# Kernel tuning notes

Measured on AMD Instinct MI355X. Metric: run time of the kernel, lower is better.

Reference implementation:

```python
import jax, jax.numpy as jnp
import numpy as np

TEMPERATURE = 0.07
EPS = 1e-12  # F.normalize clamp


def _project(x, We, be, W1, b1, W2, b2):
    # encoder Linear then projection head Linear->ReLU->Linear
    h = x @ We + be                      # [B, 512]
    h = jax.nn.relu(h @ W1 + b1)         # [B, 256]
    return h @ W2 + b2                   # [B, 128]


def _ntxent(z1, z2, t):
    B = z1.shape[0]
    z1 = z1 / jnp.maximum(jnp.linalg.norm(z1, axis=1, keepdims=True), EPS)
    z2 = z2 / jnp.maximum(jnp.linalg.norm(z2, axis=1, keepdims=True), EPS)
    reps = jnp.concatenate([z1, z2], axis=0)          # [2B, 128]
    sim = reps @ reps.T                               # [2B, 2B]
    N = 2 * B
    idx = jnp.arange(N)
    # positives: eye rolled by B along columns -> column (i+B) mod N
    pos = sim[idx, (idx + B) % N][:, None]            # [N, 1]
    # negatives: all off-diagonal entries per row, in column order
    cols = jnp.arange(N - 1)[None, :]                 # [1, N-1]
    neg_idx = cols + (cols >= idx[:, None])           # skip the diagonal
    neg = jnp.take_along_axis(sim, neg_idx, axis=1)   # [N, N-1]
    logits = jnp.concatenate([pos, neg], axis=1) / t  # [N, N]
    # cross-entropy with label 0
    return jnp.mean(jax.nn.logsumexp(logits, axis=1) - logits[:, 0])


def setup_inputs() -> dict:
    key = jax.random.key(0)
    ks = jax.random.split(key, 10)
    B, Din, Denc, Dh, Dp = 4096, 1024, 512, 256, 128
    s = lambda fan_in: 1.0 / np.sqrt(fan_in)
    return {
        "x_image": jax.random.normal(ks[0], (B, Din), jnp.float32),
        "x_text": jax.random.normal(ks[1], (B, Din), jnp.float32),
        "We_img": jax.random.normal(ks[2], (Din, Denc), jnp.float32) * s(Din),
        "be_img": jnp.zeros((Denc,), jnp.float32),
        "We_txt": jax.random.normal(ks[3], (Din, Denc), jnp.float32) * s(Din),
        "be_txt": jnp.zeros((Denc,), jnp.float32),
        "Wp1_img": jax.random.normal(ks[4], (Denc, Dh), jnp.float32) * s(Denc),
        "bp1_img": jnp.zeros((Dh,), jnp.float32),
        "Wp2_img": jax.random.normal(ks[5], (Dh, Dp), jnp.float32) * s(Dh),
        "bp2_img": jnp.zeros((Dp,), jnp.float32),
        "Wp1_txt": jax.random.normal(ks[6], (Denc, Dh), jnp.float32) * s(Denc),
        "bp1_txt": jnp.zeros((Dh,), jnp.float32),
        "Wp2_txt": jax.random.normal(ks[7], (Dh, Dp), jnp.float32) * s(Dh),
        "bp2_txt": jnp.zeros((Dp,), jnp.float32),
    }


def reference(x_image, x_text, We_img, be_img, We_txt, be_txt,
              Wp1_img, bp1_img, Wp2_img, bp2_img,
              Wp1_txt, bp1_txt, Wp2_txt, bp2_txt):
    z1 = _project(x_image, We_img, be_img, Wp1_img, bp1_img, Wp2_img, bp2_img)
    z2 = _project(x_text, We_txt, be_txt, Wp1_txt, bp1_txt, Wp2_txt, bp2_txt)
    # single modality pair ('image','text') -> one NT-Xent loss
    return _ntxent(z1, z2, TEMPERATURE)
```

## Files before the change

kernel.cpp:

```cpp
#include <hip/hip_runtime.h>
#include <hip/hip_bf16.h>
#include <math.h>

typedef __bf16 bf16_t;
typedef __bf16 bf8 __attribute__((ext_vector_type(8)));
typedef __bf16 bf4 __attribute__((ext_vector_type(4)));
typedef __bf16 bf16x2 __attribute__((ext_vector_type(2)));
typedef float f32x4 __attribute__((ext_vector_type(4)));

#define AS1 __attribute__((address_space(1)))
#define AS3 __attribute__((address_space(3)))

#define B_ROWS 4096
#define NTOT   8192
#define DIN    1024
#define DENC   512
#define DH     256
#define DP     128
#define NSLICE 16
#define INV_T        14.285714285714286f
#define SCALE_LOG2   20.609929155556620f

__device__ __forceinline__ f32x4 mfma_16x16x32(bf8 a, bf8 b, f32x4 c) {
  return __builtin_amdgcn_mfma_f32_16x16x32_bf16(a, b, c, 0, 0, 0);
}

__global__ __launch_bounds__(256) void prep_kernel(
    const float* __restrict__ x_i, const float* __restrict__ x_t,
    const float* __restrict__ We_i, const float* __restrict__ We_t,
    const float* __restrict__ W1_i, const float* __restrict__ W1_t,
    const float* __restrict__ W2_i, const float* __restrict__ W2_t,
    bf16_t* __restrict__ xb_i, bf16_t* __restrict__ xb_t,
    bf16_t* __restrict__ Wet_i, bf16_t* __restrict__ Wet_t,
    bf16_t* __restrict__ W1t_i, bf16_t* __restrict__ W1t_t,
    bf16_t* __restrict__ W2t_i, bf16_t* __restrict__ W2t_t,
    int* __restrict__ Ctr) {
  const int b = blockIdx.x;
  const int tid = threadIdx.x;
  if (b >= 336) {
    int idx = (b - 336) * 256 + tid;
    const int HALF = (B_ROWS * DIN) / 4;
    const float* s; bf16_t* d; int off;
    if (idx < HALF) { s = x_i; d = xb_i; off = idx; }
    else            { s = x_t; d = xb_t; off = idx - HALF; }
    float4 v = ((const float4*)s)[off];
    bf4 w = { (bf16_t)v.x, (bf16_t)v.y, (bf16_t)v.z, (bf16_t)v.w };
    ((bf4*)d)[off] = w;
    return;
  }
  if (b == 0 && tid < 2) Ctr[tid] = 0;
  const float* src; bf16_t* dst; int K, N, tile;
  if (b < 128)      { src = We_i; dst = Wet_i; K = 1024; N = 512; tile = b; }
  else if (b < 256) { src = We_t; dst = Wet_t; K = 1024; N = 512; tile = b - 128; }
  else if (b < 288) { src = W1_i; dst = W1t_i; K = 512;  N = 256; tile = b - 256; }
  else if (b < 320) { src = W1_t; dst = W1t_t; K = 512;  N = 256; tile = b - 288; }
  else if (b < 328) { src = W2_i; dst = W2t_i; K = 256;  N = 128; tile = b - 320; }
  else              { src = W2_t; dst = W2t_t; K = 256;  N = 128; tile = b - 328; }
  const int tilesN = N >> 6;
  const int k0 = (tile / tilesN) * 64;
  const int n0 = (tile % tilesN) * 64;

  __shared__ float ld[64][65];
  #pragma unroll
  for (int i = 0; i < 4; ++i) {
    int cid = tid + i * 256;
    int r = cid >> 4;
    int c = (cid & 15) * 4;
    float4 v = *(const float4*)(src + (size_t)(k0 + r) * N + n0 + c);
    ld[r][c + 0] = v.x; ld[r][c + 1] = v.y; ld[r][c + 2] = v.z; ld[r][c + 3] = v.w;
  }
  __syncthreads();
  #pragma unroll
  for (int i = 0; i < 2; ++i) {
    int cid = tid + i * 256;
    int rn = cid >> 3;
    int c8 = (cid & 7) * 8;
    bf8 w;
    #pragma unroll
    for (int j = 0; j < 8; ++j) w[j] = (bf16_t)ld[c8 + j][rn];
    *(bf8*)(dst + (size_t)(n0 + rn) * K + k0 + c8) = w;
  }
}

template<int MT, bool RELU>
__global__ __launch_bounds__(256) void gemm_glds(
    const bf16_t* __restrict__ A0, const bf16_t* __restrict__ A1,
    const bf16_t* __restrict__ B0, const bf16_t* __restrict__ B1,
    const float* __restrict__ bias0, const float* __restrict__ bias1,
    bf16_t* __restrict__ out0, bf16_t* __restrict__ out1,
    int N, int K) {
  const bf16_t* A   = blockIdx.z ? A1 : A0;
  const bf16_t* Bt  = blockIdx.z ? B1 : B0;
  const float* bias = blockIdx.z ? bias1 : bias0;
  bf16_t* outp      = blockIdx.z ? out1 : out0;

  const int nb   = blockIdx.x * 64;
  const int mb   = blockIdx.y * MT;
  const int tid  = threadIdx.x;
  const int wave = tid >> 6;
  const int lane = tid & 63;
  const int l15  = lane & 15;
  const int quad = lane >> 4;
  constexpr int CH = MT / 64;

  __shared__ __align__(16) bf16_t As[2][MT * 32];
  __shared__ __align__(16) bf16_t Bs[2][64 * 32];

  f32x4 acc[CH][4];
  #pragma unroll
  for (int i = 0; i < CH; ++i)
    #pragma unroll
    for (int j = 0; j < 4; ++j) acc[i][j] = (f32x4){0.f, 0.f, 0.f, 0.f};

  auto stage = [&](int k0, int pb) {
    #pragma unroll
    for (int i = 0; i < CH; ++i) {
      const int s = tid + i * 256;
      const bf16_t* ga = A + (size_t)(mb + (s >> 2)) * K + k0 + (s & 3) * 8;
      __builtin_amdgcn_global_load_lds(
          (const AS1 void*)ga,
          (AS3 void*)(As[pb] + (size_t)(wave * 64 + i * 256) * 8), 16, 0, 0);
    }
    const bf16_t* gb = Bt + (size_t)(nb + (tid >> 2)) * K + k0 + (tid & 3) * 8;
    __builtin_amdgcn_global_load_lds(
        (const AS1 void*)gb,
        (AS3 void*)(Bs[pb] + (size_t)(wave * 64) * 8), 16, 0, 0);
  };

  stage(0, 0);
  const int T = K >> 5;
  for (int t = 0; t < T; ++t) {
    __syncthreads();
    if (t + 1 < T) stage((t + 1) << 5, (t + 1) & 1);
    const bf16_t* as = As[t & 1];
    const bf16_t* bs = Bs[t & 1];
    bf8 a[CH];
    #pragma unroll
    for (int i = 0; i < CH; ++i)
      a[i] = *(const bf8*)(as + (size_t)(wave * (16 * CH) + i * 16 + l15) * 32 + quad * 8);
    #pragma unroll
    for (int nt = 0; nt < 4; ++nt) {
      bf8 bb = *(const bf8*)(bs + (size_t)(nt * 16 + l15) * 32 + quad * 8);
      #pragma unroll
      for (int i = 0; i < CH; ++i)
        acc[i][nt] = mfma_16x16x32(a[i], bb, acc[i][nt]);
    }
  }

  #pragma unroll
  for (int i = 0; i < CH; ++i) {
    const int orow = mb + wave * (16 * CH) + i * 16 + quad * 4;
    #pragma unroll
    for (int nt = 0; nt < 4; ++nt) {
      const int ocol = nb + nt * 16 + l15;
      const float bval = bias[ocol];
      #pragma unroll
      for (int r = 0; r < 4; ++r) {
        float v = acc[i][nt][r] + bval;
        if (RELU) v = fmaxf(v, 0.f);
        outp[(size_t)(orow + r) * N + ocol] = (bf16_t)v;
      }
    }
  }
}

__global__ __launch_bounds__(256) void head2_norm(
    const bf16_t* __restrict__ A0, const bf16_t* __restrict__ A1,
    const bf16_t* __restrict__ B0, const bf16_t* __restrict__ B1,
    const float* __restrict__ bias0, const float* __restrict__ bias1,
    bf16_t* __restrict__ reps) {
  const bf16_t* A   = blockIdx.z ? A1 : A0;
  const bf16_t* Bt  = blockIdx.z ? B1 : B0;
  const float* bias = blockIdx.z ? bias1 : bias0;

  const int mb   = blockIdx.x * 64;
  const int tid  = threadIdx.x;
  const int wave = tid >> 6;
  const int lane = tid & 63;
  const int l15  = lane & 15;
  const int quad = lane >> 4;

  __shared__ __align__(16) bf16_t As[64][40];
  __shared__ __align__(16) bf16_t Bs[128][40];

  f32x4 acc[8];
  #pragma unroll
  for (int i = 0; i < 8; ++i) acc[i] = (f32x4){0.f, 0.f, 0.f, 0.f};

  const int arow   = tid >> 2;
  const int achunk = (tid & 3) << 3;
  const bf16_t* Ap = A + (size_t)(mb + arow) * DH + achunk;

  for (int k0 = 0; k0 < DH; k0 += 32) {
    uint4 av = *(const uint4*)(Ap + k0);
    uint4 bv[2];
    #pragma unroll
    for (int i = 0; i < 2; ++i) {
      int cid = tid + i * 256;
      int br = cid >> 2, bc = (cid & 3) << 3;
      bv[i] = *(const uint4*)(Bt + (size_t)br * DH + k0 + bc);
    }
    __syncthreads();
    *(uint4*)&As[arow][achunk] = av;
    #pragma unroll
    for (int i = 0; i < 2; ++i) {
      int cid = tid + i * 256;
      int br = cid >> 2, bc = (cid & 3) << 3;
      *(uint4*)&Bs[br][bc] = bv[i];
    }
    __syncthreads();
    bf8 af = *(const bf8*)&As[wave * 16 + l15][quad * 8];
    #pragma unroll
    for (int nt = 0; nt < 8; ++nt) {
      bf8 bfv = *(const bf8*)&Bs[nt * 16 + l15][quad * 8];
      acc[nt] = mfma_16x16x32(af, bfv, acc[nt]);
    }
  }

  #pragma unroll
  for (int nt = 0; nt < 8; ++nt) {
    const float bval = bias[nt * 16 + l15];
    #pragma unroll
    for (int r = 0; r < 4; ++r) acc[nt][r] += bval;
  }
  const size_t rowbase = (size_t)(blockIdx.z ? B_ROWS : 0) + mb + wave * 16 + quad * 4;
  #pragma unroll
  for (int r = 0; r < 4; ++r) {
    float ss = 0.f;
    #pragma unroll
    for (int nt = 0; nt < 8; ++nt) ss += acc[nt][r] * acc[nt][r];
    ss += __shfl_xor(ss, 1);
    ss += __shfl_xor(ss, 2);
    ss += __shfl_xor(ss, 4);
    ss += __shfl_xor(ss, 8);
    const float inv = 1.0f / fmaxf(sqrtf(ss), 1e-12f);
    #pragma unroll
    for (int nt = 0; nt < 8; ++nt)
      reps[(rowbase + r) * DP + nt * 16 + l15] = (bf16_t)(acc[nt][r] * inv);
  }
}

__global__ __launch_bounds__(256) void sim_rowsum_kernel(
    const bf16_t* __restrict__ reps, float* __restrict__ Spart) {
  const int rowbase = blockIdx.y * 128;
  const int slice   = blockIdx.x;
  const int col0    = slice * 512;
  const int tid  = threadIdx.x;
  const int wave = tid >> 6;
  const int lane = tid & 63;
  const int l15  = lane & 15;
  const int quad = lane >> 4;

  __shared__ __align__(16) bf16_t Bs[2][64 * DP];

  const int r0 = rowbase + wave * 32;
  bf8 af0[4], af1[4];
  #pragma unroll
  for (int kt = 0; kt < 4; ++kt) {
    af0[kt] = *(const bf8*)(reps + (size_t)(r0 + l15)      * DP + kt * 32 + quad * 8);
    af1[kt] = *(const bf8*)(reps + (size_t)(r0 + 16 + l15) * DP + kt * 32 + quad * 8);
  }

  float rs0[4] = {0.f, 0.f, 0.f, 0.f};
  float rs1[4] = {0.f, 0.f, 0.f, 0.f};

  for (int t = 0; t < 8; ++t) {
    bf16_t* buf = Bs[t & 1];
    __syncthreads();
    const int jt0 = col0 + t * 64;
    #pragma unroll
    for (int r = 0; r < 4; ++r) {
      const int s   = r * 256 + tid;
      const int col = s >> 4;
      const int cf  = (s & 15) ^ (col & 15);
      const bf16_t* g = reps + (size_t)(jt0 + col) * DP + cf * 8;
      __builtin_amdgcn_global_load_lds(
          (const AS1 void*)g,
          (AS3 void*)(buf + (size_t)(r * 256 + wave * 64) * 8), 16, 0, 0);
    }
    __syncthreads();

    #pragma unroll
    for (int st = 0; st < 4; ++st) {
      const bf16_t* base = buf + (size_t)(st * 16 + l15) * DP;
      bf8 b0 = *(const bf8*)(base + (((0 * 4 + quad) ^ l15) * 8));
      bf8 b1 = *(const bf8*)(base + (((1 * 4 + quad) ^ l15) * 8));
      bf8 b2 = *(const bf8*)(base + (((2 * 4 + quad) ^ l15) * 8));
      bf8 b3 = *(const bf8*)(base + (((3 * 4 + quad) ^ l15) * 8));
      f32x4 acc0 = (f32x4){0.f, 0.f, 0.f, 0.f};
      f32x4 acc1 = (f32x4){0.f, 0.f, 0.f, 0.f};
      acc0 = mfma_16x16x32(af0[0], b0, acc0); acc1 = mfma_16x16x32(af1[0], b0, acc1);
      acc0 = mfma_16x16x32(af0[1], b1, acc0); acc1 = mfma_16x16x32(af1[1], b1, acc1);
      acc0 = mfma_16x16x32(af0[2], b2, acc0); acc1 = mfma_16x16x32(af1[2], b2, acc1);
      acc0 = mfma_16x16x32(af0[3], b3, acc0); acc1 = mfma_16x16x32(af1[3], b3, acc1);
      #pragma unroll
      for (int r = 0; r < 4; ++r) {
        rs0[r] += __builtin_amdgcn_exp2f(acc0[r] * SCALE_LOG2);
        rs1[r] += __builtin_amdgcn_exp2f(acc1[r] * SCALE_LOG2);
      }
    }
  }

  const int i0 = r0 + quad * 4;
  #pragma unroll
  for (int r = 0; r < 4; ++r) {
    float v = rs0[r];
    v += __shfl_xor(v, 1); v += __shfl_xor(v, 2);
    v += __shfl_xor(v, 4); v += __shfl_xor(v, 8);
    if (l15 == 0) Spart[(size_t)slice * NTOT + i0 + r] = v;
  }
  #pragma unroll
  for (int r = 0; r < 4; ++r) {
    float v = rs1[r];
    v += __shfl_xor(v, 1); v += __shfl_xor(v, 2);
    v += __shfl_xor(v, 4); v += __shfl_xor(v, 8);
    if (l15 == 0) Spart[(size_t)slice * NTOT + i0 + 16 + r] = v;
  }
}

__global__ __launch_bounds__(256) void rowfinal_kernel(
    const bf16_t* __restrict__ reps, const float* __restrict__ Spart,
    int* __restrict__ cnt, float* __restrict__ Lsum,
    float* __restrict__ out) {
  const int tid  = threadIdx.x;
  const int wave = tid >> 6;
  const int lane = tid & 63;
  float part = 0.f;
  #pragma unroll 1
  for (int i = 0; i < 16; ++i) {
    const int row = blockIdx.x * 64 + wave * 16 + i;
    bf16x2 a = *(const bf16x2*)(reps + (size_t)row * DP + lane * 2);
    bf16x2 b = *(const bf16x2*)(reps + (size_t)(row ^ B_ROWS) * DP + lane * 2);
    float a0 = (float)a.x, a1 = (float)a.y;
    float b0 = (float)b.x, b1 = (float)b.y;
    float dii = a0 * a0 + a1 * a1;
    float pos = a0 * b0 + a1 * b1;
    float ps  = (lane < NSLICE) ? Spart[(size_t)lane * NTOT + row] : 0.f;
    #pragma unroll
    for (int m = 1; m < 64; m <<= 1) {
      dii += __shfl_xor(dii, m);
      pos += __shfl_xor(pos, m);
      ps  += __shfl_xor(ps, m);
    }
    if (lane == 0) {
      float Si = ps - __builtin_amdgcn_exp2f(dii * SCALE_LOG2)
                    + __builtin_amdgcn_exp2f(pos * SCALE_LOG2);
      part += logf(Si) - pos * INV_T;
    }
  }
  __shared__ float wpart[4];
  if (lane == 0) wpart[wave] = part;
  __syncthreads();
  if (tid == 0) {
    float bsum = wpart[0] + wpart[1] + wpart[2] + wpart[3];
    atomicAdd(Lsum, bsum);
    __threadfence();
    int old = __hip_atomic_fetch_add(cnt, 1, __ATOMIC_ACQ_REL,
                                     __HIP_MEMORY_SCOPE_AGENT);
    if (old == (int)gridDim.x - 1) {
      float tot = __hip_atomic_load(Lsum, __ATOMIC_RELAXED,
                                    __HIP_MEMORY_SCOPE_AGENT);
      out[0] = tot * (1.0f / NTOT);
    }
  }
}

extern "C" void kernel_launch(void* const* d_in, const int* in_sizes, int n_in,
                              void* d_out, int out_size, void* d_ws, size_t ws_size,
                              hipStream_t stream) {
  const float* x_img  = (const float*)d_in[0];
  const float* x_txt  = (const float*)d_in[1];
  const float* We_img = (const float*)d_in[2];
  const float* be_img = (const float*)d_in[3];
  const float* We_txt = (const float*)d_in[4];
  const float* be_txt = (const float*)d_in[5];
  const float* W1_img = (const float*)d_in[6];
  const float* b1_img = (const float*)d_in[7];
  const float* W2_img = (const float*)d_in[8];
  const float* b2_img = (const float*)d_in[9];
  const float* W1_txt = (const float*)d_in[10];
  const float* b1_txt = (const float*)d_in[11];
  const float* W2_txt = (const float*)d_in[12];
  const float* b2_txt = (const float*)d_in[13];

  char* p = (char*)d_ws;
  bf16_t* xbf_img = (bf16_t*)p; p += (size_t)B_ROWS * DIN * 2;
  bf16_t* xbf_txt = (bf16_t*)p; p += (size_t)B_ROWS * DIN * 2;
  bf16_t* Wet_img = (bf16_t*)p; p += (size_t)DENC * DIN * 2;
  bf16_t* Wet_txt = (bf16_t*)p; p += (size_t)DENC * DIN * 2;
  bf16_t* W1t_img = (bf16_t*)p; p += (size_t)DH * DENC * 2;
  bf16_t* W1t_txt = (bf16_t*)p; p += (size_t)DH * DENC * 2;
  bf16_t* W2t_img = (bf16_t*)p; p += (size_t)DP * DH * 2;
  bf16_t* W2t_txt = (bf16_t*)p; p += (size_t)DP * DH * 2;
  bf16_t* h_img   = (bf16_t*)p; p += (size_t)B_ROWS * DENC * 2;
  bf16_t* h_txt   = (bf16_t*)p; p += (size_t)B_ROWS * DENC * 2;
  bf16_t* g_img   = (bf16_t*)p; p += (size_t)B_ROWS * DH * 2;
  bf16_t* g_txt   = (bf16_t*)p; p += (size_t)B_ROWS * DH * 2;
  bf16_t* reps    = (bf16_t*)p; p += (size_t)NTOT * DP * 2;
  float*  Spart   = (float*) p; p += (size_t)NSLICE * NTOT * 4;
  int*    Ctr     = (int*)   p; p += 2 * 4;

  prep_kernel<<<336 + 8192, 256, 0, stream>>>(
      x_img, x_txt, We_img, We_txt, W1_img, W1_txt, W2_img, W2_txt,
      xbf_img, xbf_txt, Wet_img, Wet_txt, W1t_img, W1t_txt, W2t_img, W2t_txt,
      Ctr);

  gemm_glds<128, false><<<dim3(DENC / 64, B_ROWS / 128, 2), 256, 0, stream>>>(
      xbf_img, xbf_txt, Wet_img, Wet_txt, be_img, be_txt, h_img, h_txt,
      DENC, DIN);
  gemm_glds<64, true><<<dim3(DH / 64, B_ROWS / 64, 2), 256, 0, stream>>>(
      h_img, h_txt, W1t_img, W1t_txt, b1_img, b1_txt, g_img, g_txt,
      DH, DENC);
  head2_norm<<<dim3(B_ROWS / 64, 1, 2), 256, 0, stream>>>(
      g_img, g_txt, W2t_img, W2t_txt, b2_img, b2_txt, reps);

  sim_rowsum_kernel<<<dim3(NSLICE, NTOT / 128), 256, 0, stream>>>(reps, Spart);
  rowfinal_kernel<<<NTOT / 64, 256, 0, stream>>>(
      reps, Spart, &Ctr[0], (float*)&Ctr[1], (float*)d_out);
}
```

Baseline: 187.7 us.

## Pipeline head2 and sim loads via global_load_lds, move diag/pos corrections into sim

head2_norm now uses 16-row blocks with four times as many blocks, splits columns across waves, and stages tiles with double-buffered direct global-to-LDS loads. The row norm is reduced across waves through shared memory. sim_rowsum_kernel prefetches the next column tile while computing the current one. The diagonal and positive-pair corrections move into the sim blocks that own those columns, which writes a Pos array, so rowfinal becomes a simple per-thread sum over slices. The aim is to raise head2 parallelism, hide load latency, and shrink rowfinal, at the cost of extra serial work in a few sim blocks.

```diff
diff --git a/kernel.cpp b/kernel.cpp
--- a/kernel.cpp
+++ b/kernel.cpp
@@ -173,75 +173,85 @@
   const bf16_t* Bt  = blockIdx.z ? B1 : B0;
   const float* bias = blockIdx.z ? bias1 : bias0;
 
-  const int mb   = blockIdx.x * 64;
+  const int mb   = blockIdx.x * 16;
   const int tid  = threadIdx.x;
   const int wave = tid >> 6;
   const int lane = tid & 63;
   const int l15  = lane & 15;
   const int quad = lane >> 4;
-
-  __shared__ __align__(16) bf16_t As[64][40];
-  __shared__ __align__(16) bf16_t Bs[128][40];
-
-  f32x4 acc[8];
-  #pragma unroll
-  for (int i = 0; i < 8; ++i) acc[i] = (f32x4){0.f, 0.f, 0.f, 0.f};
-
-  const int arow   = tid >> 2;
-  const int achunk = (tid & 3) << 3;
-  const bf16_t* Ap = A + (size_t)(mb + arow) * DH + achunk;
-
-  for (int k0 = 0; k0 < DH; k0 += 32) {
-    uint4 av = *(const uint4*)(Ap + k0);
-    uint4 bv[2];
+  const int wc0  = wave * 32;
+
+  __shared__ __align__(16) bf16_t Asb[2][16 * 32];
+  __shared__ __align__(16) bf16_t Bsb[2][128 * 32];
+  __shared__ float ssL[64];
+
+  f32x4 acc[2];
+  acc[0] = (f32x4){0.f, 0.f, 0.f, 0.f};
+  acc[1] = (f32x4){0.f, 0.f, 0.f, 0.f};
+
+  auto stage = [&](int k0, int pb) {
+    if (wave == 0) {
+      const int row = lane >> 2, j = lane & 3, cf = j ^ (row & 3);
+      const bf16_t* ga = A + (size_t)(mb + row) * DH + k0 + cf * 8;
+      __builtin_amdgcn_global_load_lds(
+          (const AS1 void*)ga, (AS3 void*)(Asb[pb]), 16, 0, 0);
+    }
     #pragma unroll
     for (int i = 0; i < 2; ++i) {
-      int cid = tid + i * 256;
-      int br = cid >> 2, bc = (cid & 3) << 3;
-      bv[i] = *(const uint4*)(Bt + (size_t)br * DH + k0 + bc);
-    }
+      const int s = wave * 64 + i * 256 + lane;
+      const int col = s >> 2, j = s & 3, cf = j ^ (col & 3);
+      const bf16_t* gb = Bt + (size_t)col * DH + k0 + cf * 8;
+      __builtin_amdgcn_global_load_lds(
+          (const AS1 void*)gb,
+          (AS3 void*)(Bsb[pb] + (size_t)(wave * 64 + i * 256) * 8), 16, 0, 0);
+    }
+  };
+
+  stage(0, 0);
+  for (int t = 0; t < 8; ++t) {
     __syncthreads();
-    *(uint4*)&As[arow][achunk] = av;
-    #pragma unroll
-    for (int i = 0; i < 2; ++i) {
-      int cid = tid + i * 256;
-      int br = cid >> 2, bc = (cid & 3) << 3;
-      *(uint4*)&Bs[br][bc] = bv[i];
-    }
-    __syncthreads();
-    bf8 af = *(const bf8*)&As[wave * 16 + l15][quad * 8];
-    #pragma unroll
-    for (int nt = 0; nt < 8; ++nt) {
-      bf8 bfv = *(const bf8*)&Bs[nt * 16 + l15][quad * 8];
-      acc[nt] = mfma_16x16x32(af, bfv, acc[nt]);
-    }
-  }
-
-  #pragma unroll
-  for (int nt = 0; nt < 8; ++nt) {
-    const float bval = bias[nt * 16 + l15];
-    #pragma unroll
-    for (int r = 0; r < 4; ++r) acc[nt][r] += bval;
-  }
-  const size_t rowbase = (size_t)(blockIdx.z ? B_ROWS : 0) + mb + wave * 16 + quad * 4;
+    if (t < 7) stage((t + 1) << 5, (t + 1) & 1);
+    const bf16_t* as = Asb[t & 1];
+    const bf16_t* bs = Bsb[t & 1];
+    bf8 a = *(const bf8*)(as + (size_t)(l15 * 4 + (quad ^ (l15 & 3))) * 8);
+    #pragma unroll
+    for (int nt = 0; nt < 2; ++nt) {
+      const int col = wc0 + nt * 16 + l15;
+      bf8 bb = *(const bf8*)(bs + (size_t)(col * 4 + (quad ^ (col & 3))) * 8);
+      acc[nt] = mfma_16x16x32(a, bb, acc[nt]);
+    }
+  }
+
+  float ssp[4];
   #pragma unroll
   for (int r = 0; r < 4; ++r) {
-    float ss = 0.f;
-    #pragma unroll
-    for (int nt = 0; nt < 8; ++nt) ss += acc[nt][r] * acc[nt][r];
-    ss += __shfl_xor(ss, 1);
-    ss += __shfl_xor(ss, 2);
-    ss += __shfl_xor(ss, 4);
-    ss += __shfl_xor(ss, 8);
-    const float inv = 1.0f / fmaxf(sqrtf(ss), 1e-12f);
-    #pragma unroll
-    for (int nt = 0; nt < 8; ++nt)
-      reps[(rowbase + r) * DP + nt * 16 + l15] = (bf16_t)(acc[nt][r] * inv);
+    #pragma unroll
+    for (int nt = 0; nt < 2; ++nt) acc[nt][r] += bias[wc0 + nt * 16 + l15];
+    float s = acc[0][r] * acc[0][r] + acc[1][r] * acc[1][r];
+    s += __shfl_xor(s, 1); s += __shfl_xor(s, 2);
+    s += __shfl_xor(s, 4); s += __shfl_xor(s, 8);
+    ssp[r] = s;
+  }
+  if (l15 == 0) {
+    #pragma unroll
+    for (int r = 0; r < 4; ++r) ssL[wave * 16 + quad * 4 + r] = ssp[r];
+  }
+  __syncthreads();
+  const size_t gr0 = (size_t)(blockIdx.z ? B_ROWS : 0) + mb + quad * 4;
+  #pragma unroll
+  for (int r = 0; r < 4; ++r) {
+    const int row = quad * 4 + r;
+    float tot = ssL[row] + ssL[16 + row] + ssL[32 + row] + ssL[48 + row];
+    const float inv = 1.0f / fmaxf(sqrtf(tot), 1e-12f);
+    #pragma unroll
+    for (int nt = 0; nt < 2; ++nt)
+      reps[(gr0 + r) * DP + wc0 + nt * 16 + l15] = (bf16_t)(acc[nt][r] * inv);
   }
 }
 
 __global__ __launch_bounds__(256) void sim_rowsum_kernel(
-    const bf16_t* __restrict__ reps, float* __restrict__ Spart) {
+    const bf16_t* __restrict__ reps, float* __restrict__ Spart,
+    float* __restrict__ Pos) {
   const int rowbase = blockIdx.y * 128;
   const int slice   = blockIdx.x;
   const int col0    = slice * 512;
@@ -264,9 +274,7 @@
   float rs0[4] = {0.f, 0.f, 0.f, 0.f};
   float rs1[4] = {0.f, 0.f, 0.f, 0.f};
 
-  for (int t = 0; t < 8; ++t) {
-    bf16_t* buf = Bs[t & 1];
-    __syncthreads();
+  auto stage = [&](int t, int pb) {
     const int jt0 = col0 + t * 64;
     #pragma unroll
     for (int r = 0; r < 4; ++r) {
@@ -276,10 +284,15 @@
       const bf16_t* g = reps + (size_t)(jt0 + col) * DP + cf * 8;
       __builtin_amdgcn_global_load_lds(
           (const AS1 void*)g,
-          (AS3 void*)(buf + (size_t)(r * 256 + wave * 64) * 8), 16, 0, 0);
-    }
+          (AS3 void*)(Bs[pb] + (size_t)(r * 256 + wave * 64) * 8), 16, 0, 0);
+    }
+  };
+
+  stage(0, 0);
+  for (int t = 0; t < 8; ++t) {
     __syncthreads();
-
+    if (t < 7) stage(t + 1, (t + 1) & 1);
+    const bf16_t* buf = Bs[t & 1];
     #pragma unroll
     for (int st = 0; st < 4; ++st) {
       const bf16_t* base = buf + (size_t)(st * 16 + l15) * DP;
@@ -301,6 +314,33 @@
     }
   }
 
+  const bool isDiag = (slice == (rowbase >> 9));
+  const bool isPos  = (slice == ((rowbase ^ B_ROWS) >> 9));
+  if (isDiag || isPos) {
+    #pragma unroll 1
+    for (int i = 0; i < 32; ++i) {
+      const int row = r0 + i;
+      bf16x2 av = *(const bf16x2*)(reps + (size_t)row * DP + lane * 2);
+      float a0 = (float)av.x, a1 = (float)av.y;
+      float dv;
+      if (isDiag) {
+        dv = a0 * a0 + a1 * a1;
+      } else {
+        bf16x2 bv = *(const bf16x2*)(reps + (size_t)(row ^ B_ROWS) * DP + lane * 2);
+        dv = a0 * (float)bv.x + a1 * (float)bv.y;
+      }
+      #pragma unroll
+      for (int m = 1; m < 64; m <<= 1) dv += __shfl_xor(dv, m);
+      const float e = __builtin_amdgcn_exp2f(dv * SCALE_LOG2);
+      const float corr = isDiag ? -e : e;
+      const int q = (i & 15) >> 2, r = i & 3;
+      if (l15 == 0 && quad == q) {
+        if (i < 16) rs0[r] += corr; else rs1[r] += corr;
+      }
+      if (isPos && lane == 0) Pos[row] = dv;
+    }
+  }
+
   const int i0 = r0 + quad * 4;
   #pragma unroll
   for (int r = 0; r < 4; ++r) {
@@ -319,37 +359,19 @@
 }
 
 __global__ __launch_bounds__(256) void rowfinal_kernel(
-    const bf16_t* __restrict__ reps, const float* __restrict__ Spart,
+    const float* __restrict__ Spart, const float* __restrict__ Pos,
     int* __restrict__ cnt, float* __restrict__ Lsum,
     float* __restrict__ out) {
-  const int tid  = threadIdx.x;
-  const int wave = tid >> 6;
-  const int lane = tid & 63;
-  float part = 0.f;
-  #pragma unroll 1
-  for (int i = 0; i < 16; ++i) {
-    const int row = blockIdx.x * 64 + wave * 16 + i;
-    bf16x2 a = *(const bf16x2*)(reps + (size_t)row * DP + lane * 2);
-    bf16x2 b = *(const bf16x2*)(reps + (size_t)(row ^ B_ROWS) * DP + lane * 2);
-    float a0 = (float)a.x, a1 = (float)a.y;
-    float b0 = (float)b.x, b1 = (float)b.y;
-    float dii = a0 * a0 + a1 * a1;
-    float pos = a0 * b0 + a1 * b1;
-    float ps  = (lane < NSLICE) ? Spart[(size_t)lane * NTOT + row] : 0.f;
-    #pragma unroll
-    for (int m = 1; m < 64; m <<= 1) {
-      dii += __shfl_xor(dii, m);
-      pos += __shfl_xor(pos, m);
-      ps  += __shfl_xor(ps, m);
-    }
-    if (lane == 0) {
-      float Si = ps - __builtin_amdgcn_exp2f(dii * SCALE_LOG2)
-                    + __builtin_amdgcn_exp2f(pos * SCALE_LOG2);
-      part += logf(Si) - pos * INV_T;
-    }
-  }
+  const int tid = threadIdx.x;
+  const int row = blockIdx.x * 256 + tid;
+  float s = 0.f;
+  #pragma unroll
+  for (int k = 0; k < NSLICE; ++k) s += Spart[(size_t)k * NTOT + row];
+  float L = logf(s) - Pos[row] * INV_T;
+  #pragma unroll
+  for (int m = 1; m < 64; m <<= 1) L += __shfl_xor(L, m);
   __shared__ float wpart[4];
-  if (lane == 0) wpart[wave] = part;
+  if ((tid & 63) == 0) wpart[tid >> 6] = L;
   __syncthreads();
   if (tid == 0) {
     float bsum = wpart[0] + wpart[1] + wpart[2] + wpart[3];
@@ -398,6 +420,7 @@
   bf16_t* g_txt   = (bf16_t*)p; p += (size_t)B_ROWS * DH * 2;
   bf16_t* reps    = (bf16_t*)p; p += (size_t)NTOT * DP * 2;
   float*  Spart   = (float*) p; p += (size_t)NSLICE * NTOT * 4;
+  float*  Pos     = (float*) p; p += (size_t)NTOT * 4;
   int*    Ctr     = (int*)   p; p += 2 * 4;
 
   prep_kernel<<<336 + 8192, 256, 0, stream>>>(
@@ -411,10 +434,11 @@
   gemm_glds<64, true><<<dim3(DH / 64, B_ROWS / 64, 2), 256, 0, stream>>>(
       h_img, h_txt, W1t_img, W1t_txt, b1_img, b1_txt, g_img, g_txt,
       DH, DENC);
-  head2_norm<<<dim3(B_ROWS / 64, 1, 2), 256, 0, stream>>>(
+  head2_norm<<<dim3(B_ROWS / 16, 1, 2), 256, 0, stream>>>(
       g_img, g_txt, W2t_img, W2t_txt, b2_img, b2_txt, reps);
 
-  sim_rowsum_kernel<<<dim3(NSLICE, NTOT / 128), 256, 0, stream>>>(reps, Spart);
-  rowfinal_kernel<<<NTOT / 64, 256, 0, stream>>>(
-      reps, Spart, &Ctr[0], (float*)&Ctr[1], (float*)d_out);
-}
+  sim_rowsum_kernel<<<dim3(NSLICE, NTOT / 128), 256, 0, stream>>>(
+      reps, Spart, Pos);
+  rowfinal_kernel<<<NTOT / 256, 256, 0, stream>>>(
+      Spart, Pos, &Ctr[0], (float*)&Ctr[1], (float*)d_out);
+}
```

After: 187.3 us. About the same (-0.2%).
